# Kernel tuning notes

Hardware: AMD Instinct MI355X
Metric: run time of the kernel (lower is better)

Reference implementation:

```python
import jax, jax.numpy as jnp
import numpy as np

DIM = 1024
HEADS = 16
DIM_HEAD = 64
INNER = HEADS * DIM_HEAD  # 1024
EPS = 1e-5


def layernorm(x, w, b):
    mu = jnp.mean(x, axis=-1, keepdims=True)
    var = jnp.mean(jnp.square(x - mu), axis=-1, keepdims=True)
    return (x - mu) * jax.lax.rsqrt(var + EPS) * w + b


def setup_inputs() -> dict:
    key = jax.random.key(0)
    ks = jax.random.split(key, 9)
    b, n1, n2 = 4, 4096, 256
    x = jax.random.normal(ks[0], (b, n1, DIM), dtype=jnp.float32)
    latents = jax.random.normal(ks[1], (b, n2, DIM), dtype=jnp.float32)
    shift = jax.random.normal(ks[2], (b, HEADS), dtype=jnp.float32)
    scale = jax.random.normal(ks[3], (b, HEADS), dtype=jnp.float32)
    s = 1.0 / np.sqrt(DIM)
    Wq = jax.random.normal(ks[4], (DIM, INNER), dtype=jnp.float32) * s
    Wkv = jax.random.normal(ks[5], (DIM, 2 * INNER), dtype=jnp.float32) * s
    Wout = jax.random.normal(ks[6], (INNER, DIM), dtype=jnp.float32) * (1.0 / np.sqrt(INNER))
    ln1_w = jnp.ones((DIM,), jnp.float32)
    ln1_b = jnp.zeros((DIM,), jnp.float32)
    ln2_w = jnp.ones((DIM,), jnp.float32)
    ln2_b = jnp.zeros((DIM,), jnp.float32)
    return {"x": x, "latents": latents, "shift": shift, "scale": scale,
            "ln1_w": ln1_w, "ln1_b": ln1_b, "ln2_w": ln2_w, "ln2_b": ln2_b,
            "Wq": Wq, "Wkv": Wkv, "Wout": Wout}


def reference(x, latents, shift, scale, ln1_w, ln1_b, ln2_w, ln2_b, Wq, Wkv, Wout):
    b = x.shape[0]
    xn = layernorm(x, ln1_w, ln1_b)            # (b, n1, D)
    ln = layernorm(latents, ln2_w, ln2_b)      # (b, n2, D)
    q = ln @ Wq                                 # (b, n2, inner)
    kv = xn @ Wkv                               # (b, n1, 2*inner)
    k, v = jnp.split(kv, 2, axis=-1)
    q = q.reshape(b, -1, HEADS, DIM_HEAD)
    k = k.reshape(b, -1, HEADS, DIM_HEAD)
    v = v.reshape(b, -1, HEADS, DIM_HEAD)
    # AdaLN-style per-head modulation on q
    q = q * (1.0 + scale[:, None, :, None]) + shift[:, None, :, None]
    # fp32 attention scores (already fp32 here)
    attn_scale = DIM_HEAD ** -0.5
    qk = jnp.einsum('bihd,bjhd->bhij', q.astype(jnp.float32), k.astype(jnp.float32)) * attn_scale
    attn = jax.nn.softmax(qk, axis=-1).astype(v.dtype)  # (b, h, n2, n1)
    out = jnp.einsum('bhij,bjhd->bihd', attn, v)         # (b, n2, h, dh)
    out = out.reshape(b, -1, INNER)
    return out @ Wout
```

## Files before the change

kernel.cpp:

```cpp
#include <hip/hip_runtime.h>

typedef __bf16 bf16;
typedef bf16 bf16x8 __attribute__((ext_vector_type(8)));
typedef bf16 bf16x4 __attribute__((ext_vector_type(4)));
typedef float f32x4 __attribute__((ext_vector_type(4)));

#define B_ 4
#define N1 4096
#define N2 256
#define DIM 1024
#define HEADS 16
#define DH 64
#define INNER 1024
#define ASPLIT 4
#define KEYS_PER_SPLIT (N1 / ASPLIT)
#define SPLIT_ELEMS (4 * 16 * 256 * 64)
#define ROWS_TOTAL (4 * HEADS * N2)

typedef __attribute__((address_space(1))) const void gvoid_t;
typedef __attribute__((address_space(3))) void lvoid_t;
__device__ __forceinline__ void async16(const void* g, void* l) {
  __builtin_amdgcn_global_load_lds((gvoid_t*)g, (lvoid_t*)l, 16, 0, 0);
}

__global__ __launch_bounds__(256) void prep(
    const float* __restrict__ Wq, const float* __restrict__ Wkv,
    const float* __restrict__ Wout, bf16* __restrict__ WqT,
    bf16* __restrict__ WkvT, bf16* __restrict__ WoutT,
    const float* __restrict__ x, const float* __restrict__ latents,
    const float* __restrict__ ln1w, const float* __restrict__ ln1b,
    const float* __restrict__ ln2w, const float* __restrict__ ln2b,
    bf16* __restrict__ xn, bf16* __restrict__ lnl) {
  __shared__ float tile[32][33];
  int t = blockIdx.x;
  if (t < 4096) {
    const float* src;
    bf16* dst;
    int N;
    if (t < 1024) { src = Wq; dst = WqT; N = 1024; }
    else if (t < 3072) { t -= 1024; src = Wkv; dst = WkvT; N = 2048; }
    else { t -= 3072; src = Wout; dst = WoutT; N = 1024; }
    int ntiles = N >> 5;
    int n0 = (t % ntiles) * 32, k0 = (t / ntiles) * 32;
    int xx = threadIdx.x & 31, yy = threadIdx.x >> 5;
    for (int j = 0; j < 4; j++)
      tile[yy + 8 * j][xx] = src[(size_t)(k0 + yy + 8 * j) * N + n0 + xx];
    __syncthreads();
    for (int j = 0; j < 4; j++)
      dst[(size_t)(n0 + yy + 8 * j) * 1024 + k0 + xx] = (bf16)tile[xx][yy + 8 * j];
    return;
  }
  int wv = threadIdx.x >> 6, lane = threadIdx.x & 63;
  int grow = (t - 4096) * 4 + wv;
  const float *src, *w, *bb;
  bf16* dst;
  int row;
  if (grow < 16384) { src = x; w = ln1w; bb = ln1b; dst = xn; row = grow; }
  else { src = latents; w = ln2w; bb = ln2b; dst = lnl; row = grow - 16384; }
  const float4* p = (const float4*)(src + (size_t)row * DIM);
  float4 v[4];
  for (int j = 0; j < 4; j++) v[j] = p[j * 64 + lane];
  float s = 0.f, sq = 0.f;
  for (int j = 0; j < 4; j++) {
    s += v[j].x + v[j].y + v[j].z + v[j].w;
    sq += v[j].x * v[j].x + v[j].y * v[j].y + v[j].z * v[j].z + v[j].w * v[j].w;
  }
  for (int off = 32; off; off >>= 1) {
    s += __shfl_xor(s, off, 64);
    sq += __shfl_xor(sq, off, 64);
  }
  float mu = s * (1.0f / DIM);
  float var = sq * (1.0f / DIM) - mu * mu;
  float r = rsqrtf(var + 1e-5f);
  for (int j = 0; j < 4; j++) {
    float4 wv4 = ((const float4*)w)[j * 64 + lane];
    float4 bv4 = ((const float4*)bb)[j * 64 + lane];
    bf16x4 o;
    o[0] = (bf16)((v[j].x - mu) * r * wv4.x + bv4.x);
    o[1] = (bf16)((v[j].y - mu) * r * wv4.y + bv4.y);
    o[2] = (bf16)((v[j].z - mu) * r * wv4.z + bv4.z);
    o[3] = (bf16)((v[j].w - mu) * r * wv4.w + bv4.w);
    *(bf16x4*)(dst + (size_t)row * DIM + (j * 64 + lane) * 4) = o;
  }
}

__device__ __forceinline__ int swz_off(int row, int cb) {
  int line = row >> 1;
  return (line << 7) + (((((row & 1) << 2) | cb) ^ (line & 7)) << 4);
}

__global__ __launch_bounds__(512, 2) void gemm_kv256(
    const bf16* __restrict__ A, const bf16* __restrict__ Bt,
    bf16* __restrict__ Cout, bf16* __restrict__ Cout2,
    const bf16* __restrict__ Aq, const bf16* __restrict__ Bq,
    bf16* __restrict__ qout, const float* __restrict__ shiftp,
    const float* __restrict__ scalep) {
  extern __shared__ char smem[];
  int tid = threadIdx.x;
  int lane = tid & 63, wv = tid >> 6;
  int lr = lane & 15, quad = lane >> 4;
  int bid = blockIdx.x;

  if (bid >= 512) {
    int q2 = bid - 512;
    int m0q = (q2 >> 4) * 64, n0q = (q2 & 15) * 64;
    int wrq = wv >> 1, wcq = wv & 1;
    int srow = tid >> 3;
    int scb = (tid & 7) ^ (srow & 7);
    size_t ga = (size_t)(m0q + srow) * 1024 + scb * 8;
    size_t gb = (size_t)(n0q + srow) * 1024 + scb * 8;
    int ldsW = wv * 1024;
    auto stq = [&](int step, int buf) {
      int kt = step * 64;
      async16(&Aq[ga + kt], smem + buf * 8192 + ldsW);
      async16(&Bq[gb + kt], smem + 24576 + buf * 8192 + ldsW);
    };
    f32x4 accq[2] = {};
    stq(0, 0);
    stq(1, 1);
    asm volatile("s_waitcnt vmcnt(2)" ::: "memory");
    __builtin_amdgcn_s_barrier();
#pragma unroll 1
    for (int s = 0; s < 16; s++) {
      int cur = s % 3;
      int nxt = (s + 2 < 16) ? s + 2 : 15;
      stq(nxt, (s + 2) % 3);
      const bf16* Ab = (const bf16*)(smem + cur * 8192);
      const bf16* Bb = (const bf16*)(smem + 24576 + cur * 8192);
      for (int kk = 0; kk < 2; kk++) {
        int arow = wrq * 16 + lr;
        bf16x8 afq =
            *(const bf16x8*)&Ab[arow * 64 + ((4 * kk + quad) ^ (arow & 7)) * 8];
        for (int in = 0; in < 2; in++) {
          int brow = wcq * 32 + in * 16 + lr;
          bf16x8 bfq =
              *(const bf16x8*)&Bb[brow * 64 + ((4 * kk + quad) ^ (brow & 7)) * 8];
          accq[in] = __builtin_amdgcn_mfma_f32_16x16x32_bf16(afq, bfq, accq[in],
                                                             0, 0, 0);
        }
      }
      asm volatile("s_waitcnt vmcnt(2)" ::: "memory");
      __builtin_amdgcn_s_barrier();
    }
    for (int in = 0; in < 2; in++) {
      int col = n0q + wcq * 32 + in * 16 + lr;
      int hh = col >> 6;
      for (int r = 0; r < 4; r++) {
        int row = m0q + wrq * 16 + quad * 4 + r;
        int bb = row >> 8;
        float sc = scalep[bb * 16 + hh], sh = shiftp[bb * 16 + hh];
        qout[(size_t)row * 1024 + col] =
            (bf16)((accq[in][r] * (1.0f + sc) + sh) * 0.18033688011112042f);
      }
    }
    return;
  }

  int wr = wv >> 2, wc = wv & 3;
  int mt = (bid & 7) * 8 + ((bid >> 3) >> 3), nt = (bid >> 3) & 7;
  int m0 = mt * 256, n0 = nt * 256;

  int offA[8], offB[4];
#pragma unroll
  for (int im = 0; im < 8; im++) offA[im] = swz_off(wr * 128 + im * 16 + lr, quad);
#pragma unroll
  for (int in = 0; in < 4; in++) offB[in] = swz_off(wc * 64 + in * 16 + lr, quad);

  size_t gA[2], gB[2];
#pragma unroll
  for (int s = 0; s < 2; s++) {
    int u = s * 512 + tid;
    int line = u >> 3, inner = (u & 7) ^ (line & 7);
    int row = line * 2 + (inner >> 2), cb = inner & 3;
    gA[s] = (size_t)(m0 + row) * 1024 + cb * 8;
    gB[s] = (size_t)(n0 + row) * 1024 + cb * 8;
  }
  int ldsS0 = wv * 1024, ldsS1 = 8192 + wv * 1024;

  auto stA = [&](int b, int kh, int k0) {
    char* base = smem + b * 32768 + kh * 16384;
    async16(&A[gA[0] + k0], base + ldsS0);
    async16(&A[gA[1] + k0], base + ldsS1);
  };
  auto stB = [&](int b, int kh, int k0) {
    char* base = smem + 65536 + b * 32768 + kh * 16384;
    async16(&Bt[gB[0] + k0], base + ldsS0);
    async16(&Bt[gB[1] + k0], base + ldsS1);
  };

  f32x4 acc[8][4] = {};

  stA(0, 0, 0);  stB(0, 0, 0);
  stA(0, 1, 32); stB(0, 1, 32);
  stA(1, 0, 64); stB(1, 0, 64);
  asm volatile("s_waitcnt vmcnt(4)" ::: "memory");
  __builtin_amdgcn_s_barrier();

#pragma unroll 1
  for (int t = 0; t < 16; t++) {
    int b = t & 1;
    const char* A0 = smem + b * 32768;
    const char* A1 = A0 + 16384;
    const char* B0 = smem + 65536 + b * 32768;
    const char* B1 = B0 + 16384;
    int k1 = (t + 1 < 16 ? t + 1 : 15) * 64;
    int k2 = (t + 2 < 16 ? t + 2 : 15) * 64;
    bf16x8 af[4], bfr[4];
#pragma unroll
    for (int in = 0; in < 4; in++) bfr[in] = *(const bf16x8*)(B0 + offB[in]);
#pragma unroll
    for (int im = 0; im < 4; im++) af[im] = *(const bf16x8*)(A0 + offA[im]);
    stA(b ^ 1, 1, k1 + 32);
    __builtin_amdgcn_s_barrier();
    __builtin_amdgcn_s_setprio(1);
#pragma unroll
    for (int im = 0; im < 4; im++)
#pragma unroll
      for (int in = 0; in < 4; in++)
        acc[im][in] = __builtin_amdgcn_mfma_f32_16x16x32_bf16(
            af[im], bfr[in], acc[im][in], 0, 0, 0);
    __builtin_amdgcn_s_setprio(0);
    __builtin_amdgcn_s_barrier();
#pragma unroll
    for (int im = 0; im < 4; im++) af[im] = *(const bf16x8*)(A0 + offA[4 + im]);
    stB(b ^ 1, 1, k1 + 32);
    __builtin_amdgcn_s_barrier();
    __builtin_amdgcn_s_setprio(1);
#pragma unroll
    for (int im = 0; im < 4; im++)
#pragma unroll
      for (int in = 0; in < 4; in++)
        acc[4 + im][in] = __builtin_amdgcn_mfma_f32_16x16x32_bf16(
            af[im], bfr[in], acc[4 + im][in], 0, 0, 0);
    __builtin_amdgcn_s_setprio(0);
    __builtin_amdgcn_s_barrier();
#pragma unroll
    for (int in = 0; in < 4; in++) bfr[in] = *(const bf16x8*)(B1 + offB[in]);
#pragma unroll
    for (int im = 0; im < 4; im++) af[im] = *(const bf16x8*)(A1 + offA[im]);
    stA(b, 0, k2);
    __builtin_amdgcn_s_barrier();
    __builtin_amdgcn_s_setprio(1);
#pragma unroll
    for (int im = 0; im < 4; im++)
#pragma unroll
      for (int in = 0; in < 4; in++)
        acc[im][in] = __builtin_amdgcn_mfma_f32_16x16x32_bf16(
            af[im], bfr[in], acc[im][in], 0, 0, 0);
    __builtin_amdgcn_s_setprio(0);
    __builtin_amdgcn_s_barrier();
#pragma unroll
    for (int im = 0; im < 4; im++) af[im] = *(const bf16x8*)(A1 + offA[4 + im]);
    stB(b, 0, k2);
    __builtin_amdgcn_s_barrier();
    __builtin_amdgcn_s_setprio(1);
#pragma unroll
    for (int im = 0; im < 4; im++)
#pragma unroll
      for (int in = 0; in < 4; in++)
        acc[4 + im][in] = __builtin_amdgcn_mfma_f32_16x16x32_bf16(
            af[im], bfr[in], acc[4 + im][in], 0, 0, 0);
    __builtin_amdgcn_s_setprio(0);
    asm volatile("s_waitcnt vmcnt(4)" ::: "memory");
    __builtin_amdgcn_s_barrier();
  }

  asm volatile("s_waitcnt vmcnt(0)" ::: "memory");
  __builtin_amdgcn_s_barrier();

  if (n0 < 1024) {
#pragma unroll
    for (int im = 0; im < 8; im++)
#pragma unroll
      for (int in = 0; in < 4; in++) {
        int col = n0 + wc * 64 + in * 16 + lr;
#pragma unroll
        for (int r = 0; r < 4; r++) {
          int row = m0 + wr * 128 + im * 16 + quad * 4 + r;
          Cout[(size_t)row * 1024 + col] = (bf16)acc[im][in][r];
        }
      }
    return;
  }
  int b2 = m0 >> 12;
  int key0 = (m0 & 4095) + wr * 128;
  int gc0 = (n0 - 1024) + wc * 64;
  bf16* Tw = (bf16*)(smem + wv * 8704);
  for (int pass = 0; pass < 2; pass++) {
#pragma unroll
    for (int ii = 0; ii < 2; ii++) {
      int in = pass * 2 + ii;
      int cl = ii * 16 + lr;
#pragma unroll
      for (int im = 0; im < 8; im++) {
        bf16x4 pk;
#pragma unroll
        for (int r = 0; r < 4; r++) pk[r] = (bf16)acc[im][in][r];
        *(bf16x4*)&Tw[cl * 136 + im * 16 + quad * 4] = pk;
      }
    }
    asm volatile("s_waitcnt lgkmcnt(0)" ::: "memory");
#pragma unroll
    for (int j = 0; j < 8; j++) {
      int idx = j * 64 + lane;
      int cl = idx >> 4, k8 = idx & 15;
      uint4 val = *(const uint4*)&Tw[cl * 136 + k8 * 8];
      *(uint4*)&Cout2[((size_t)(b2 * 1024 + gc0 + pass * 32 + cl)) * 4096 +
                      key0 + k8 * 8] = val;
    }
    asm volatile("s_waitcnt lgkmcnt(0)" ::: "memory");
  }
}

template <int MODE>
__global__ __launch_bounds__(256) void gemm64(
    const bf16* __restrict__ A, const bf16* __restrict__ Bt,
    void* __restrict__ Cout, int K, int N,
    const float* __restrict__ shiftp, const float* __restrict__ scalep) {
  __shared__ __align__(16) bf16 As[3][64 * 64];
  __shared__ __align__(16) bf16 Bs[3][64 * 64];
  int tid = threadIdx.x;
  int lane = tid & 63, wv = tid >> 6;
  int wr = wv >> 1, wc = wv & 1;
  int quad = lane >> 4, lr = lane & 15;
  int m0 = blockIdx.y * 64, n0 = blockIdx.x * 64;
  f32x4 acc[2][2] = {};

  auto stage = [&](int step, int buf) {
    int kt = step * 64;
    for (int j = 0; j < 2; j++) {
      int idx0 = j * 256 + wv * 64;
      int row = (idx0 >> 3) + (lane >> 3);
      int cb = (lane & 7) ^ (row & 7);
      async16(&A[(size_t)(m0 + row) * K + kt + cb * 8], &As[buf][idx0 * 8]);
      async16(&Bt[(size_t)(n0 + row) * K + kt + cb * 8], &Bs[buf][idx0 * 8]);
    }
  };

  int nsteps = K >> 6;
  stage(0, 0);
  stage(1, 1);
  asm volatile("s_waitcnt vmcnt(4)" ::: "memory");
  __builtin_amdgcn_s_barrier();

#pragma unroll 1
  for (int s = 0; s < nsteps; s++) {
    int cur = s % 3;
    int nxt = (s + 2 < nsteps) ? s + 2 : nsteps - 1;
    stage(nxt, (s + 2) % 3);
    for (int kk = 0; kk < 2; kk++) {
      bf16x8 af[2], bfr[2];
      for (int im = 0; im < 2; im++) {
        int row = wr * 32 + im * 16 + lr;
        af[im] =
            *(const bf16x8*)&As[cur][row * 64 + ((quad + 4 * kk) ^ (row & 7)) * 8];
      }
      for (int in = 0; in < 2; in++) {
        int row = wc * 32 + in * 16 + lr;
        bfr[in] =
            *(const bf16x8*)&Bs[cur][row * 64 + ((quad + 4 * kk) ^ (row & 7)) * 8];
      }
      for (int im = 0; im < 2; im++)
        for (int in = 0; in < 2; in++)
          acc[im][in] = __builtin_amdgcn_mfma_f32_16x16x32_bf16(
              af[im], bfr[in], acc[im][in], 0, 0, 0);
    }
    asm volatile("s_waitcnt vmcnt(4)" ::: "memory");
    __builtin_amdgcn_s_barrier();
  }

  for (int im = 0; im < 2; im++)
    for (int in = 0; in < 2; in++) {
      int col = n0 + wc * 32 + in * 16 + lr;
      for (int r = 0; r < 4; r++) {
        int row = m0 + wr * 32 + im * 16 + quad * 4 + r;
        float v = acc[im][in][r];
        if (MODE == 1) {
          int bb = row >> 8, hh = col >> 6;
          float sc = scalep[bb * 16 + hh], sh = shiftp[bb * 16 + hh];
          ((bf16*)Cout)[(size_t)row * N + col] =
              (bf16)((v * (1.0f + sc) + sh) * 0.18033688011112042f);
        } else {
          ((float*)Cout)[(size_t)row * N + col] = v;
        }
      }
    }
}

__global__ __launch_bounds__(512) void attn_kernel(const bf16* __restrict__ q,
                                                   const bf16* __restrict__ kb,
                                                   const bf16* __restrict__ vt,
                                                   bf16* __restrict__ opb,
                                                   float* __restrict__ lseb) {
  int b = blockIdx.z, h = blockIdx.y;
  int sp = blockIdx.x;
  int tid = threadIdx.x, lane = tid & 63, wv = tid >> 6;
  int quad = lane >> 4, lr = lane & 15;
  __shared__ __align__(16) bf16 Ks[2][64 * 64];
  __shared__ __align__(16) bf16 Vs[2][64 * 64];
  __shared__ __align__(16) bf16 QP[256 * 64];

  const bf16* qg = q + (size_t)(b * N2) * INNER + h * DH;
  for (int j = 0; j < 4; j++) {
    int r0 = j * 64 + wv * 8;
    int r = r0 + (lane >> 3);
    async16(&qg[(size_t)r * INNER + ((lane & 7) ^ (r & 7)) * 8], &QP[r0 * 64]);
  }
  __syncthreads();
  bf16x8 aQ[2][2];
  for (int g = 0; g < 2; g++) {
    int row = wv * 32 + g * 16 + lr;
    for (int kk = 0; kk < 2; kk++)
      aQ[g][kk] = *(const bf16x8*)&QP[row * 64 + ((quad + 4 * kk) ^ (row & 7)) * 8];
  }
  float m_s[2] = {-1e30f, -1e30f}, l_s[2] = {0.0f, 0.0f};
  f32x4 oacc[2][4] = {};

  const bf16* kg = kb + (size_t)(b * N1) * 1024 + h * DH;
  const bf16* vg = vt + (size_t)((b * HEADS + h) * DH) * N1;
  bf16* Ps = QP + wv * 2048;

  auto stageKV = [&](int t, int buf) {
    int key0 = sp * KEYS_PER_SPLIT + t * 64;
    int r0 = wv * 8;
    int r = r0 + (lane >> 3);
    int cs = ((lane & 7) ^ (r & 7)) * 8;
    async16(&kg[(size_t)(key0 + r) * 1024 + cs], &Ks[buf][r0 * 64]);
    async16(&vg[(size_t)r * N1 + key0 + cs], &Vs[buf][r0 * 64]);
  };

  stageKV(0, 0);
  asm volatile("s_waitcnt vmcnt(0)" ::: "memory");
  __builtin_amdgcn_s_barrier();

  for (int t = 0; t < KEYS_PER_SPLIT / 64; t++) {
    int cur = t & 1;
    bf16x8 ak[2][4], bv[2][4];
    for (int kk = 0; kk < 2; kk++)
      for (int nt = 0; nt < 4; nt++) {
        int row = nt * 16 + lr;
        ak[kk][nt] =
            *(const bf16x8*)&Ks[cur][row * 64 + ((quad + 4 * kk) ^ (row & 7)) * 8];
        bv[kk][nt] =
            *(const bf16x8*)&Vs[cur][row * 64 + ((quad + 4 * kk) ^ (row & 7)) * 8];
      }
    if (t + 1 < KEYS_PER_SPLIT / 64) stageKV(t + 1, cur ^ 1);

    for (int g = 0; g < 2; g++) {
      f32x4 s[4] = {};
      for (int kk = 0; kk < 2; kk++)
        for (int nt = 0; nt < 4; nt++)
          s[nt] = __builtin_amdgcn_mfma_f32_16x16x32_bf16(ak[kk][nt], aQ[g][kk],
                                                          s[nt], 0, 0, 0);
      float mx = s[0][0];
      for (int nt = 0; nt < 4; nt++)
        for (int r = 0; r < 4; r++) mx = fmaxf(mx, s[nt][r]);
      mx = fmaxf(mx, __shfl_xor(mx, 16, 64));
      mx = fmaxf(mx, __shfl_xor(mx, 32, 64));
      float mo = m_s[g];
      float mn = fmaxf(mo, mx);
      float al = exp2f(mo - mn);
      float p[4][4], sum = 0.0f;
      for (int nt = 0; nt < 4; nt++)
        for (int r = 0; r < 4; r++) {
          p[nt][r] = exp2f(s[nt][r] - mn);
          sum += p[nt][r];
        }
      sum += __shfl_xor(sum, 16, 64);
      sum += __shfl_xor(sum, 32, 64);
      l_s[g] = l_s[g] * al + sum;
      m_s[g] = mn;

      for (int nt = 0; nt < 4; nt++) {
        bf16x4 pk;
        for (int r = 0; r < 4; r++) pk[r] = (bf16)p[nt][r];
        *(bf16x4*)&Ps[lr * 64 + ((2 * nt + (quad >> 1)) ^ (lr & 7)) * 8 +
                      (quad & 1) * 4] = pk;
      }

      if (__any(mn > mo)) {
        for (int r = 0; r < 4; r++) {
          float a = __shfl(al, quad * 4 + r, 16);
          for (int in = 0; in < 4; in++) oacc[g][in][r] *= a;
        }
      }

      bf16x8 aP[2];
      for (int kk = 0; kk < 2; kk++)
        aP[kk] = *(const bf16x8*)&Ps[lr * 64 + ((4 * kk + quad) ^ (lr & 7)) * 8];
      for (int kk = 0; kk < 2; kk++)
        for (int in = 0; in < 4; in++)
          oacc[g][in] = __builtin_amdgcn_mfma_f32_16x16x32_bf16(
              aP[kk], bv[kk][in], oacc[g][in], 0, 0, 0);
    }
    asm volatile("s_waitcnt vmcnt(0)" ::: "memory");
    __builtin_amdgcn_s_barrier();
  }

  bf16* ob = opb + (size_t)sp * SPLIT_ELEMS;
  size_t rbase = (size_t)(b * HEADS + h) * N2;
  for (int g = 0; g < 2; g++) {
    for (int r = 0; r < 4; r++) {
      float lrow = __shfl(l_s[g], quad * 4 + r, 16);
      float inv = 1.0f / lrow;
      int qq = wv * 32 + g * 16 + quad * 4 + r;
      for (int in = 0; in < 4; in++)
        ob[(rbase + qq) * 64 + in * 16 + lr] = (bf16)(oacc[g][in][r] * inv);
    }
    if (quad == 0) {
      int qq = wv * 32 + g * 16 + lr;
      lseb[(size_t)sp * ROWS_TOTAL + rbase + qq] = m_s[g] + __log2f(l_s[g]);
    }
  }
}

__global__ __launch_bounds__(256) void combine_kernel(const bf16* __restrict__ opb,
                                                      const float* __restrict__ lseb,
                                                      bf16* __restrict__ out) {
  int gid = blockIdx.x * 256 + threadIdx.x;
  int dc = (gid & 7) * 8;
  int rq = gid >> 3;
  int qq = rq & 255, bh = rq >> 8;
  int h = bh & 15, b = bh >> 4;
  float ls[ASPLIT];
  for (int s = 0; s < ASPLIT; s++) ls[s] = lseb[(size_t)s * ROWS_TOTAL + rq];
  float M = fmaxf(fmaxf(ls[0], ls[1]), fmaxf(ls[2], ls[3]));
  float L = 0.0f, w[ASPLIT];
  for (int s = 0; s < ASPLIT; s++) {
    w[s] = exp2f(ls[s] - M);
    L += w[s];
  }
  float inv = 1.0f / L;
  float o[8] = {};
  for (int s = 0; s < ASPLIT; s++) {
    bf16x8 v = *(const bf16x8*)&opb[(size_t)s * SPLIT_ELEMS + (size_t)rq * 64 + dc];
    for (int j = 0; j < 8; j++) o[j] += w[s] * (float)v[j];
  }
  bf16x8 ov;
  for (int j = 0; j < 8; j++) ov[j] = (bf16)(o[j] * inv);
  *(bf16x8*)&out[((size_t)(b * N2 + qq)) * INNER + h * DH + dc] = ov;
}

extern "C" void kernel_launch(void* const* d_in, const int* in_sizes, int n_in,
                              void* d_out, int out_size, void* d_ws,
                              size_t ws_size, hipStream_t stream) {
  const float* x       = (const float*)d_in[0];
  const float* latents = (const float*)d_in[1];
  const float* shift   = (const float*)d_in[2];
  const float* scale   = (const float*)d_in[3];
  const float* ln1w    = (const float*)d_in[4];
  const float* ln1b    = (const float*)d_in[5];
  const float* ln2w    = (const float*)d_in[6];
  const float* ln2b    = (const float*)d_in[7];
  const float* Wq      = (const float*)d_in[8];
  const float* Wkv     = (const float*)d_in[9];
  const float* Wout    = (const float*)d_in[10];

  char* ws = (char*)d_ws;
  bf16*  xn    = (bf16*)(ws);
  bf16*  opb   = (bf16*)(ws);
  bf16*  lnl   = (bf16*)(ws + 33554432);
  float* lseb  = (float*)(ws + 33554432);
  bf16*  qb    = (bf16*)(ws + 35651584);
  bf16*  kb    = (bf16*)(ws + 37748736);
  bf16*  vtb   = (bf16*)(ws + 104857600);
  bf16*  aob   = (bf16*)(ws + 138412032);
  bf16*  WqT   = (bf16*)(ws + 140509184);
  bf16*  WkvT  = (bf16*)(ws + 142606336);
  bf16*  WoutT = (bf16*)(ws + 146800640);

  static bool attr_done = false;
  if (!attr_done) {
    hipFuncSetAttribute(reinterpret_cast<const void*>(gemm_kv256),
                        hipFuncAttributeMaxDynamicSharedMemorySize, 131072);
    attr_done = true;
  }

  prep<<<8448, 256, 0, stream>>>(Wq, Wkv, Wout, WqT, WkvT, WoutT, x, latents,
                                 ln1w, ln1b, ln2w, ln2b, xn, lnl);
  gemm_kv256<<<dim3(768), dim3(512), 131072, stream>>>(
      xn, WkvT, kb, vtb, lnl, WqT, qb, shift, scale);
  attn_kernel<<<dim3(ASPLIT, 16, 4), 512, 0, stream>>>(qb, kb, vtb, opb,
                                                       lseb);
  combine_kernel<<<512, 256, 0, stream>>>(opb, lseb, aob);
  gemm64<2><<<dim3(16, 16), 256, 0, stream>>>(aob, WoutT, d_out, 1024, 1024,
                                              nullptr, nullptr);
}
```

Baseline: 262.8 us.

## Halve KV GEMM LDS footprint with 32-wide K stages to raise occupancy

Restructures the KV/Q projection GEMM main loop from 64-wide K steps with split half-tile loads into 32 single-stage steps. Each step double-buffers combined A and B tiles, which cuts dynamic shared memory from 128 KB to about 68 KB per block. The aim is to fit more blocks per CU (launch bounds raised to 4) so latency is hidden by occupancy rather than deep in-block prefetch. The cost is more loop iterations and barriers, less prefetch lookahead, and a tighter register budget that may force spills of the 128-float accumulator.

```diff
diff --git a/kernel.cpp b/kernel.cpp
--- a/kernel.cpp
+++ b/kernel.cpp
@@ -89,7 +89,7 @@
   return (line << 7) + (((((row & 1) << 2) | cb) ^ (line & 7)) << 4);
 }
 
-__global__ __launch_bounds__(512, 2) void gemm_kv256(
+__global__ __launch_bounds__(512, 4) void gemm_kv256(
     const bf16* __restrict__ A, const bf16* __restrict__ Bt,
     bf16* __restrict__ Cout, bf16* __restrict__ Cout2,
     const bf16* __restrict__ Aq, const bf16* __restrict__ Bq,
@@ -177,40 +177,34 @@
   }
   int ldsS0 = wv * 1024, ldsS1 = 8192 + wv * 1024;
 
-  auto stA = [&](int b, int kh, int k0) {
-    char* base = smem + b * 32768 + kh * 16384;
-    async16(&A[gA[0] + k0], base + ldsS0);
-    async16(&A[gA[1] + k0], base + ldsS1);
+  auto stAB = [&](int w, int buf) {
+    int k0 = w * 32;
+    char* ba = smem + buf * 16384;
+    char* bb = smem + 32768 + buf * 16384;
+    async16(&A[gA[0] + k0], ba + ldsS0);
+    async16(&A[gA[1] + k0], ba + ldsS1);
+    async16(&Bt[gB[0] + k0], bb + ldsS0);
+    async16(&Bt[gB[1] + k0], bb + ldsS1);
   };
-  auto stB = [&](int b, int kh, int k0) {
-    char* base = smem + 65536 + b * 32768 + kh * 16384;
-    async16(&Bt[gB[0] + k0], base + ldsS0);
-    async16(&Bt[gB[1] + k0], base + ldsS1);
-  };
 
   f32x4 acc[8][4] = {};
 
-  stA(0, 0, 0);  stB(0, 0, 0);
-  stA(0, 1, 32); stB(0, 1, 32);
-  stA(1, 0, 64); stB(1, 0, 64);
+  stAB(0, 0);
+  stAB(1, 1);
   asm volatile("s_waitcnt vmcnt(4)" ::: "memory");
   __builtin_amdgcn_s_barrier();
 
 #pragma unroll 1
-  for (int t = 0; t < 16; t++) {
-    int b = t & 1;
-    const char* A0 = smem + b * 32768;
-    const char* A1 = A0 + 16384;
-    const char* B0 = smem + 65536 + b * 32768;
-    const char* B1 = B0 + 16384;
-    int k1 = (t + 1 < 16 ? t + 1 : 15) * 64;
-    int k2 = (t + 2 < 16 ? t + 2 : 15) * 64;
+  for (int s = 0; s < 32; s++) {
+    int buf = s & 1;
+    const char* A0 = smem + buf * 16384;
+    const char* B0 = smem + 32768 + buf * 16384;
+    int w2 = (s + 2 < 32) ? s + 2 : 31;
     bf16x8 af[4], bfr[4];
 #pragma unroll
     for (int in = 0; in < 4; in++) bfr[in] = *(const bf16x8*)(B0 + offB[in]);
 #pragma unroll
     for (int im = 0; im < 4; im++) af[im] = *(const bf16x8*)(A0 + offA[im]);
-    stA(b ^ 1, 1, k1 + 32);
     __builtin_amdgcn_s_barrier();
     __builtin_amdgcn_s_setprio(1);
 #pragma unroll
@@ -223,7 +217,6 @@
     __builtin_amdgcn_s_barrier();
 #pragma unroll
     for (int im = 0; im < 4; im++) af[im] = *(const bf16x8*)(A0 + offA[4 + im]);
-    stB(b ^ 1, 1, k1 + 32);
     __builtin_amdgcn_s_barrier();
     __builtin_amdgcn_s_setprio(1);
 #pragma unroll
@@ -233,34 +226,7 @@
         acc[4 + im][in] = __builtin_amdgcn_mfma_f32_16x16x32_bf16(
             af[im], bfr[in], acc[4 + im][in], 0, 0, 0);
     __builtin_amdgcn_s_setprio(0);
-    __builtin_amdgcn_s_barrier();
-#pragma unroll
-    for (int in = 0; in < 4; in++) bfr[in] = *(const bf16x8*)(B1 + offB[in]);
-#pragma unroll
-    for (int im = 0; im < 4; im++) af[im] = *(const bf16x8*)(A1 + offA[im]);
-    stA(b, 0, k2);
-    __builtin_amdgcn_s_barrier();
-    __builtin_amdgcn_s_setprio(1);
-#pragma unroll
-    for (int im = 0; im < 4; im++)
-#pragma unroll
-      for (int in = 0; in < 4; in++)
-        acc[im][in] = __builtin_amdgcn_mfma_f32_16x16x32_bf16(
-            af[im], bfr[in], acc[im][in], 0, 0, 0);
-    __builtin_amdgcn_s_setprio(0);
-    __builtin_amdgcn_s_barrier();
-#pragma unroll
-    for (int im = 0; im < 4; im++) af[im] = *(const bf16x8*)(A1 + offA[4 + im]);
-    stB(b, 0, k2);
-    __builtin_amdgcn_s_barrier();
-    __builtin_amdgcn_s_setprio(1);
-#pragma unroll
-    for (int im = 0; im < 4; im++)
-#pragma unroll
-      for (int in = 0; in < 4; in++)
-        acc[4 + im][in] = __builtin_amdgcn_mfma_f32_16x16x32_bf16(
-            af[im], bfr[in], acc[4 + im][in], 0, 0, 0);
-    __builtin_amdgcn_s_setprio(0);
+    stAB(w2, buf);
     asm volatile("s_waitcnt vmcnt(4)" ::: "memory");
     __builtin_amdgcn_s_barrier();
   }
@@ -572,13 +538,13 @@
   static bool attr_done = false;
   if (!attr_done) {
     hipFuncSetAttribute(reinterpret_cast<const void*>(gemm_kv256),
-                        hipFuncAttributeMaxDynamicSharedMemorySize, 131072);
+                        hipFuncAttributeMaxDynamicSharedMemorySize, 69632);
     attr_done = true;
   }
 
   prep<<<8448, 256, 0, stream>>>(Wq, Wkv, Wout, WqT, WkvT, WoutT, x, latents,
                                  ln1w, ln1b, ln2w, ln2b, xn, lnl);
-  gemm_kv256<<<dim3(768), dim3(512), 131072, stream>>>(
+  gemm_kv256<<<dim3(768), dim3(512), 69632, stream>>>(
       xn, WkvT, kb, vtb, lnl, WqT, qb, shift, scale);
   attn_kernel<<<dim3(ASPLIT, 16, 4), 512, 0, stream>>>(qb, kb, vtb, opb,
                                                        lseb);
```

Measured after the change: 701.0 us. 167% more time.
